# Optimization experiments

Measured on AMD Instinct MI355X. Metric: run time of the kernel, lower is better.

The kernel has to match this reference:

```python
import jax, jax.numpy as jnp
import numpy as np

HIDDEN = 2048
NUM_EXPERTS = 64
TOP_K = 8
EPS = 1e-6


def setup_inputs() -> dict:
    key = jax.random.key(0)
    k1, k2, k3, k4 = jax.random.split(key, 4)
    hidden_states = jax.random.normal(k1, (4, 4096, HIDDEN), dtype=jnp.float32)
    scale = jnp.ones((HIDDEN,), dtype=jnp.float32) + 0.01 * jax.random.normal(k2, (HIDDEN,), dtype=jnp.float32)
    proj_w = jax.random.normal(k3, (NUM_EXPERTS, HIDDEN), dtype=jnp.float32) * (HIDDEN ** -0.5)
    per_expert_scale = jnp.ones((NUM_EXPERTS,), dtype=jnp.float32) + 0.01 * jax.random.normal(k4, (NUM_EXPERTS,), dtype=jnp.float32)
    return {"hidden_states": hidden_states, "scale": scale, "proj_w": proj_w, "per_expert_scale": per_expert_scale}


def reference(hidden_states, scale, proj_w, per_expert_scale):
    H = hidden_states.shape[-1]
    # RMSNorm without learned scale
    x = hidden_states * jax.lax.rsqrt(jnp.mean(hidden_states * hidden_states, axis=-1, keepdims=True) + EPS)
    # elementwise scale and 1/sqrt(H) root-size scaling
    x = x * scale * (H ** -0.5)
    # router logits: [B,S,E]
    logits = jnp.einsum("bsh,eh->bse", x, proj_w)
    router_probs = jax.nn.softmax(logits.astype(jnp.float32), axis=-1)
    top_k_weights, top_k_index = jax.lax.top_k(router_probs, TOP_K)
    top_k_weights = top_k_weights / jnp.sum(top_k_weights, axis=-1, keepdims=True)
    top_k_weights = top_k_weights * per_expert_scale[top_k_index]
    # histc with bins=E, min=0, max=E on integer indices == bincount
    num_tokens_per_expert = jnp.bincount(top_k_index.reshape(-1), length=NUM_EXPERTS).astype(jnp.float32)
    return (top_k_weights.astype(hidden_states.dtype), top_k_index, num_tokens_per_expert)
```

## Files before the change

kernel.cpp:

```cpp
#include <hip/hip_runtime.h>
#include <math.h>

#define HIDDEN   2048
#define NEXPERT  64
#define TOPK     8
#define NTOK     16384
#define TOKB     64
#define RSQRT_H  0.02209708691207961
#define WSCALE   64.0f

typedef __attribute__((ext_vector_type(8))) _Float16       v8h;
typedef __attribute__((ext_vector_type(8))) unsigned short v8u;
typedef __attribute__((ext_vector_type(4))) float          v4f;

static __device__ __forceinline__ unsigned short f16b(float x) {
    return __builtin_bit_cast(unsigned short, (_Float16)x);
}
static __device__ __forceinline__ float f16f(unsigned short u) {
    return (float)__builtin_bit_cast(_Float16, u);
}

__global__ __launch_bounds__(256) void prep_wf(
    const float* __restrict__ w, const float* __restrict__ scale,
    unsigned short* __restrict__ wf, float* __restrict__ out_c)
{
    int i    = blockIdx.x * 256 + threadIdx.x;
    if (i < NEXPERT) out_c[i] = 0.f;
    int j    = i & 7;
    int lane = (i >> 3) & 63;
    int nt   = (i >> 9) & 3;
    int ks   = i >> 11;
    int e    = nt * 16 + (lane & 15);
    int k    = ks * 32 + (lane >> 4) * 8 + j;
    float v  = w[e * HIDDEN + k] * scale[k] * WSCALE;
    unsigned short vh = f16b(v);
    unsigned short vl = f16b(v - f16f(vh));
    size_t base = (((size_t)(ks * 4 + nt) * 2) * 64 + lane) * 8 + j;
    wf[base]       = vh;
    wf[base + 512] = vl;
}

static __device__ __forceinline__ void cvt8(
    float4 a, float4 b, v8h& ah, v8h& al, float& ss)
{
    float vv[8] = {a.x, a.y, a.z, a.w, b.x, b.y, b.z, b.w};
    v8u uh, ul;
#pragma unroll
    for (int j = 0; j < 8; ++j) {
        float v = vv[j];
        unsigned short hh = f16b(v);
        uh[j] = hh;
        ul[j] = f16b(v - f16f(hh));
        ss    = fmaf(v, v, ss);
    }
    ah = __builtin_bit_cast(v8h, uh);
    al = __builtin_bit_cast(v8h, ul);
}

__global__ __launch_bounds__(512, 1) void router_main(
    const float* __restrict__ h, const unsigned short* __restrict__ wf,
    const float* __restrict__ pes,
    float* __restrict__ out_w, float* __restrict__ out_i, float* __restrict__ out_c)
{
    __shared__ __align__(16) float lg[8 * 64 * 66];
    __shared__ float lss[8 * 64];
    __shared__ int   hist[NEXPERT];

    const int tid  = (int)threadIdx.x;
    const int w    = __builtin_amdgcn_readfirstlane(tid >> 6);
    const int lane = tid & 63;
    const int m    = lane & 15;
    const int quad = lane >> 4;
    const int t0   = (int)blockIdx.x * TOKB;

    if (tid < NEXPERT) hist[tid] = 0;

    const float* xp0 = h + (size_t)(t0 + m) * HIDDEN + w * 256 + quad * 8;
    const float* xp1 = xp0 + (size_t)16 * HIDDEN;
    const float* xp2 = xp0 + (size_t)32 * HIDDEN;
    const float* xp3 = xp0 + (size_t)48 * HIDDEN;
    const unsigned short* wq = wf + (size_t)(w * 8) * 4096 + (size_t)lane * 8;

    v4f acc[4][4];
#pragma unroll
    for (int t = 0; t < 4; ++t)
#pragma unroll
        for (int nt = 0; nt < 4; ++nt) acc[t][nt] = (v4f)0.f;
    float ss[4] = {0.f, 0.f, 0.f, 0.f};

    float4 ca[4], cb[4];
    ca[0] = *(const float4*)xp0; cb[0] = *(const float4*)(xp0 + 4);
    ca[1] = *(const float4*)xp1; cb[1] = *(const float4*)(xp1 + 4);
    ca[2] = *(const float4*)xp2; cb[2] = *(const float4*)(xp2 + 4);
    ca[3] = *(const float4*)xp3; cb[3] = *(const float4*)(xp3 + 4);

#pragma unroll
    for (int s = 0; s < 8; ++s) {
        const unsigned short* bq = wq + (size_t)s * 4096;
        v8h bh[4], bl[4];
#pragma unroll
        for (int nt = 0; nt < 4; ++nt) {
            bh[nt] = *(const v8h*)(bq + nt * 1024);
            bl[nt] = *(const v8h*)(bq + nt * 1024 + 512);
        }
        float4 na[4], nb[4];
        if (s < 7) {
            na[0] = *(const float4*)(xp0 + (s + 1) * 32);
            nb[0] = *(const float4*)(xp0 + (s + 1) * 32 + 4);
            na[1] = *(const float4*)(xp1 + (s + 1) * 32);
            nb[1] = *(const float4*)(xp1 + (s + 1) * 32 + 4);
            na[2] = *(const float4*)(xp2 + (s + 1) * 32);
            nb[2] = *(const float4*)(xp2 + (s + 1) * 32 + 4);
            na[3] = *(const float4*)(xp3 + (s + 1) * 32);
            nb[3] = *(const float4*)(xp3 + (s + 1) * 32 + 4);
        }
        __builtin_amdgcn_sched_barrier(0);

#pragma unroll
        for (int t = 0; t < 4; ++t) {
            v8h ah, al;
            cvt8(ca[t], cb[t], ah, al, ss[t]);
#pragma unroll
            for (int nt = 0; nt < 4; ++nt) {
                acc[t][nt] = __builtin_amdgcn_mfma_f32_16x16x32_f16(ah, bh[nt], acc[t][nt], 0, 0, 0);
                acc[t][nt] = __builtin_amdgcn_mfma_f32_16x16x32_f16(ah, bl[nt], acc[t][nt], 0, 0, 0);
                acc[t][nt] = __builtin_amdgcn_mfma_f32_16x16x32_f16(al, bh[nt], acc[t][nt], 0, 0, 0);
            }
        }

        if (s < 7) {
#pragma unroll
            for (int t = 0; t < 4; ++t) { ca[t] = na[t]; cb[t] = nb[t]; }
        }
    }

#pragma unroll
    for (int t = 0; t < 4; ++t) {
        float s = ss[t];
        s += __shfl_xor(s, 16, 64);
        s += __shfl_xor(s, 32, 64);
        if (lane < 16) lss[w * 64 + t * 16 + lane] = s;
    }

#pragma unroll
    for (int t = 0; t < 4; ++t)
#pragma unroll
        for (int nt = 0; nt < 4; ++nt)
#pragma unroll
            for (int r = 0; r < 4; ++r)
                lg[(w * 64 + t * 16 + quad * 4 + r) * 66 + nt * 16 + m] = acc[t][nt][r];
    __syncthreads();

    for (int i = 0; i < 8; ++i) {
        const int tok = w * 8 + i;
        float l0 = lg[(0 * 64 + tok) * 66 + lane], l1 = lg[(1 * 64 + tok) * 66 + lane];
        float l2 = lg[(2 * 64 + tok) * 66 + lane], l3 = lg[(3 * 64 + tok) * 66 + lane];
        float l4 = lg[(4 * 64 + tok) * 66 + lane], l5 = lg[(5 * 64 + tok) * 66 + lane];
        float l6 = lg[(6 * 64 + tok) * 66 + lane], l7 = lg[(7 * 64 + tok) * 66 + lane];
        float lsum = ((l0 + l1) + (l2 + l3)) + ((l4 + l5) + (l6 + l7));
        float q01 = lss[0 * 64 + tok] + lss[1 * 64 + tok];
        float q23 = lss[2 * 64 + tok] + lss[3 * 64 + tok];
        float q45 = lss[4 * 64 + tok] + lss[5 * 64 + tok];
        float q67 = lss[6 * 64 + tok] + lss[7 * 64 + tok];
        double sst = (double)((q01 + q23) + (q45 + q67));
        double rr  = 1.0 / sqrt(sst * (1.0 / (double)HIDDEN) + 1e-6);
        float logit = (float)((double)lsum * rr * (RSQRT_H / (double)WSCALE));

        float work = logit;
        float myval = 0.f; int myidx = 0; float m0 = 0.f;
#pragma unroll
        for (int j = 0; j < TOPK; ++j) {
            float mx = work;
#pragma unroll
            for (int off = 32; off; off >>= 1) mx = fmaxf(mx, __shfl_xor(mx, off, 64));
            unsigned long long msk = __ballot(work == mx);
            int src = __ffsll((long long)msk) - 1;
            if (j == 0) m0 = mx;
            if (lane == j) { myval = mx; myidx = src; }
            if (lane == src) work = -3.402823466e38f;
        }

        float ev = (lane < TOPK) ? expf(myval - m0) : 0.f;
        float es = ev;
        es += __shfl_xor(es, 1, 64);
        es += __shfl_xor(es, 2, 64);
        es += __shfl_xor(es, 4, 64);
        if (lane < TOPK) {
            float wgt = (ev / es) * pes[myidx];
            size_t o = (size_t)(t0 + tok) * TOPK + lane;
            out_w[o] = wgt;
            out_i[o] = (float)myidx;
            atomicAdd(&hist[myidx], 1);
        }
    }

    __syncthreads();
    if (tid < NEXPERT)
        atomicAdd(&out_c[tid], (float)hist[tid]);
}

extern "C" void kernel_launch(void* const* d_in, const int* in_sizes, int n_in,
                              void* d_out, int out_size, void* d_ws, size_t ws_size,
                              hipStream_t stream) {
    const float* h     = (const float*)d_in[0];
    const float* scale = (const float*)d_in[1];
    const float* w     = (const float*)d_in[2];
    const float* pes   = (const float*)d_in[3];

    unsigned short* wf = (unsigned short*)d_ws;

    float* out_w = (float*)d_out;
    float* out_i = (float*)d_out + (size_t)NTOK * TOPK;
    float* out_c = (float*)d_out + (size_t)NTOK * TOPK * 2;

    prep_wf<<<512, 256, 0, stream>>>(w, scale, wf, out_c);

    router_main<<<NTOK / TOKB, 512, 0, stream>>>(h, wf, pes, out_w, out_i, out_c);
}
```

Measured before the change: 239.3 us.

## Stage hidden-state tiles through LDS with async global_load_lds double buffering

Hidden-state loads now go through direct global-to-LDS async loads into a per-wave double-buffered, XOR-swizzled staging area, replacing register loads with a strided per-lane pattern. Weight fragments are ping-ponged between two register sets so the next step's loads overlap the current MFMA work, with explicit vmcnt waits. The logits buffer aliases the staging memory, so a barrier is added before it is overwritten. The goal is coalesced full-row loads and better latency hiding, at the cost of LDS traffic, larger shared memory use and hand-tuned waitcnt fragility.

```diff
diff --git a/kernel.cpp b/kernel.cpp
--- a/kernel.cpp
+++ b/kernel.cpp
@@ -62,23 +62,23 @@
     const float* __restrict__ pes,
     float* __restrict__ out_w, float* __restrict__ out_i, float* __restrict__ out_c)
 {
-    __shared__ __align__(16) float lg[8 * 64 * 66];
-    __shared__ float lss[8 * 64];
-    __shared__ int   hist[NEXPERT];
+    __shared__ __align__(16) char smem[137472];
+    float* stage = (float*)smem;
+    float* lg    = (float*)smem;
+    float* lss   = (float*)(smem + 135168);
+    int*   hist  = (int*)(smem + 137216);
 
     const int tid  = (int)threadIdx.x;
     const int w    = __builtin_amdgcn_readfirstlane(tid >> 6);
     const int lane = tid & 63;
     const int m    = lane & 15;
     const int quad = lane >> 4;
+    const int mq   = lane & 7;
     const int t0   = (int)blockIdx.x * TOKB;
 
     if (tid < NEXPERT) hist[tid] = 0;
 
-    const float* xp0 = h + (size_t)(t0 + m) * HIDDEN + w * 256 + quad * 8;
-    const float* xp1 = xp0 + (size_t)16 * HIDDEN;
-    const float* xp2 = xp0 + (size_t)32 * HIDDEN;
-    const float* xp3 = xp0 + (size_t)48 * HIDDEN;
+    const int swz = (((lane & 7) ^ (lane >> 3)) << 2);
     const unsigned short* wq = wf + (size_t)(w * 8) * 4096 + (size_t)lane * 8;
 
     v4f acc[4][4];
@@ -88,51 +88,77 @@
         for (int nt = 0; nt < 4; ++nt) acc[t][nt] = (v4f)0.f;
     float ss[4] = {0.f, 0.f, 0.f, 0.f};
 
-    float4 ca[4], cb[4];
-    ca[0] = *(const float4*)xp0; cb[0] = *(const float4*)(xp0 + 4);
-    ca[1] = *(const float4*)xp1; cb[1] = *(const float4*)(xp1 + 4);
-    ca[2] = *(const float4*)xp2; cb[2] = *(const float4*)(xp2 + 4);
-    ca[3] = *(const float4*)xp3; cb[3] = *(const float4*)(xp3 + 4);
-
-#pragma unroll
-    for (int s = 0; s < 8; ++s) {
-        const unsigned short* bq = wq + (size_t)s * 4096;
-        v8h bh[4], bl[4];
-#pragma unroll
-        for (int nt = 0; nt < 4; ++nt) {
-            bh[nt] = *(const v8h*)(bq + nt * 1024);
-            bl[nt] = *(const v8h*)(bq + nt * 1024 + 512);
-        }
-        float4 na[4], nb[4];
-        if (s < 7) {
-            na[0] = *(const float4*)(xp0 + (s + 1) * 32);
-            nb[0] = *(const float4*)(xp0 + (s + 1) * 32 + 4);
-            na[1] = *(const float4*)(xp1 + (s + 1) * 32);
-            nb[1] = *(const float4*)(xp1 + (s + 1) * 32 + 4);
-            na[2] = *(const float4*)(xp2 + (s + 1) * 32);
-            nb[2] = *(const float4*)(xp2 + (s + 1) * 32 + 4);
-            na[3] = *(const float4*)(xp3 + (s + 1) * 32);
-            nb[3] = *(const float4*)(xp3 + (s + 1) * 32 + 4);
-        }
-        __builtin_amdgcn_sched_barrier(0);
-
-#pragma unroll
-        for (int t = 0; t < 4; ++t) {
-            v8h ah, al;
-            cvt8(ca[t], cb[t], ah, al, ss[t]);
-#pragma unroll
-            for (int nt = 0; nt < 4; ++nt) {
-                acc[t][nt] = __builtin_amdgcn_mfma_f32_16x16x32_f16(ah, bh[nt], acc[t][nt], 0, 0, 0);
-                acc[t][nt] = __builtin_amdgcn_mfma_f32_16x16x32_f16(ah, bl[nt], acc[t][nt], 0, 0, 0);
-                acc[t][nt] = __builtin_amdgcn_mfma_f32_16x16x32_f16(al, bh[nt], acc[t][nt], 0, 0, 0);
-            }
-        }
-
-        if (s < 7) {
-#pragma unroll
-            for (int t = 0; t < 4; ++t) { ca[t] = na[t]; cb[t] = nb[t]; }
-        }
-    }
+    v8h bhA[4], blA[4], bhB[4], blB[4];
+
+#pragma unroll
+    for (int i = 0; i < 8; ++i) {
+        const float* gp = h + (size_t)(t0 + i * 8 + (lane >> 3)) * HIDDEN
+                        + w * 256 + swz;
+        __builtin_amdgcn_global_load_lds(
+            (const __attribute__((address_space(1))) void*)gp,
+            (__attribute__((address_space(3))) void*)(stage + w * 4096 + i * 256),
+            16, 0, 0);
+    }
+#pragma unroll
+    for (int nt = 0; nt < 4; ++nt) {
+        bhA[nt] = *(const v8h*)(wq + nt * 1024);
+        blA[nt] = *(const v8h*)(wq + nt * 1024 + 512);
+    }
+    __builtin_amdgcn_sched_barrier(0);
+
+#define ROUTER_STEP(S, CH, CL, NH, NL)                                        \
+    {                                                                          \
+        if ((S) < 7) {                                                         \
+            float* dst = stage + w * 4096 + (((S) + 1) & 1) * 2048;            \
+            _Pragma("unroll")                                                  \
+            for (int i = 0; i < 8; ++i) {                                      \
+                const float* gp = h + (size_t)(t0 + i * 8 + (lane >> 3)) * HIDDEN \
+                                + w * 256 + ((S) + 1) * 32 + swz;              \
+                __builtin_amdgcn_global_load_lds(                              \
+                    (const __attribute__((address_space(1))) void*)gp,         \
+                    (__attribute__((address_space(3))) void*)(dst + i * 256),  \
+                    16, 0, 0);                                                 \
+            }                                                                  \
+        }                                                                      \
+        __builtin_amdgcn_sched_barrier(0);                                     \
+        if ((S) < 7) {                                                         \
+            const unsigned short* bq = wq + (size_t)((S) + 1) * 4096;          \
+            _Pragma("unroll")                                                  \
+            for (int nt = 0; nt < 4; ++nt) {                                   \
+                NH[nt] = *(const v8h*)(bq + nt * 1024);                        \
+                NL[nt] = *(const v8h*)(bq + nt * 1024 + 512);                  \
+            }                                                                  \
+        }                                                                      \
+        __builtin_amdgcn_sched_barrier(0);                                     \
+        if ((S) < 7) asm volatile("s_waitcnt vmcnt(16)" ::: "memory");         \
+        else         asm volatile("s_waitcnt vmcnt(0)"  ::: "memory");         \
+        __builtin_amdgcn_sched_barrier(0);                                     \
+        const float* chunk = stage + w * 4096 + ((S) & 1) * 2048;              \
+        _Pragma("unroll")                                                      \
+        for (int t = 0; t < 4; ++t) {                                          \
+            const float* rb = chunk + (t * 16 + m) * 32;                       \
+            float4 va = *(const float4*)(rb + (((quad * 2) ^ mq) << 2));       \
+            float4 vb = *(const float4*)(rb + (((quad * 2 + 1) ^ mq) << 2));   \
+            v8h ah, al;                                                        \
+            cvt8(va, vb, ah, al, ss[t]);                                       \
+            _Pragma("unroll")                                                  \
+            for (int nt = 0; nt < 4; ++nt) {                                   \
+                acc[t][nt] = __builtin_amdgcn_mfma_f32_16x16x32_f16(ah, CH[nt], acc[t][nt], 0, 0, 0); \
+                acc[t][nt] = __builtin_amdgcn_mfma_f32_16x16x32_f16(ah, CL[nt], acc[t][nt], 0, 0, 0); \
+                acc[t][nt] = __builtin_amdgcn_mfma_f32_16x16x32_f16(al, CH[nt], acc[t][nt], 0, 0, 0); \
+            }                                                                  \
+        }                                                                      \
+    }
+
+    ROUTER_STEP(0, bhA, blA, bhB, blB)
+    ROUTER_STEP(1, bhB, blB, bhA, blA)
+    ROUTER_STEP(2, bhA, blA, bhB, blB)
+    ROUTER_STEP(3, bhB, blB, bhA, blA)
+    ROUTER_STEP(4, bhA, blA, bhB, blB)
+    ROUTER_STEP(5, bhB, blB, bhA, blA)
+    ROUTER_STEP(6, bhA, blA, bhB, blB)
+    ROUTER_STEP(7, bhB, blB, bhA, blA)
+#undef ROUTER_STEP
 
 #pragma unroll
     for (int t = 0; t < 4; ++t) {
@@ -141,6 +167,7 @@
         s += __shfl_xor(s, 32, 64);
         if (lane < 16) lss[w * 64 + t * 16 + lane] = s;
     }
+    __syncthreads();
 
 #pragma unroll
     for (int t = 0; t < 4; ++t)
```

Result: no change. 240.2 us (+0.4%).
